# Optimization experiments

Measured on AMD Instinct MI355X. Metric: run time of the kernel, lower is better.

The kernel has to match this reference:

```python
import jax, jax.numpy as jnp
import numpy as np

D_IN, D_HID, D_CLS, N_CLASSES = 1024, 256, 128, 4
CELL_IN = 512
N = 50000


def setup_inputs() -> dict:
    key = jax.random.key(0)
    ks = jax.random.split(key, 20)
    s = 0.02
    inp = {
        "x_path": jax.random.normal(ks[0], (1, N, D_IN), jnp.float32),
        "x_cell": jax.random.normal(ks[1], (1, N, CELL_IN), jnp.float32),
        # wsi_net / cell_net projections
        "wsi_w": jax.random.normal(ks[2], (D_IN, D_HID), jnp.float32) * s,
        "wsi_b": jnp.zeros((D_HID,), jnp.float32),
        "cell_w": jax.random.normal(ks[3], (CELL_IN, D_HID), jnp.float32) * s,
        "cell_b": jnp.zeros((D_HID,), jnp.float32),
        # cross-attention Q/K/V
        "wq_w": jax.random.normal(ks[4], (D_HID, D_HID), jnp.float32) * s,
        "wq_b": jnp.zeros((D_HID,), jnp.float32),
        "wk_w": jax.random.normal(ks[5], (D_HID, D_HID), jnp.float32) * s,
        "wk_b": jnp.zeros((D_HID,), jnp.float32),
        "wv_w": jax.random.normal(ks[6], (D_HID, D_HID), jnp.float32) * s,
        "wv_b": jnp.zeros((D_HID,), jnp.float32),
        # gated attention (L=D=256, n_classes=1)
        "aa_w": jax.random.normal(ks[7], (D_HID, D_HID), jnp.float32) * s,
        "aa_b": jnp.zeros((D_HID,), jnp.float32),
        "ab_w": jax.random.normal(ks[8], (D_HID, D_HID), jnp.float32) * s,
        "ab_b": jnp.zeros((D_HID,), jnp.float32),
        "ac_w": jax.random.normal(ks[9], (D_HID, 1), jnp.float32) * s,
        "ac_b": jnp.zeros((1,), jnp.float32),
        # classifier MLP
        "c1_w": jax.random.normal(ks[10], (D_HID, D_CLS), jnp.float32) * s,
        "c1_b": jnp.zeros((D_CLS,), jnp.float32),
        "c2_w": jax.random.normal(ks[11], (D_CLS, N_CLASSES), jnp.float32) * s,
        "c2_b": jnp.zeros((N_CLASSES,), jnp.float32),
    }
    return inp


def reference(x_path, x_cell, wsi_w, wsi_b, cell_w, cell_b,
              wq_w, wq_b, wk_w, wk_b, wv_w, wv_b,
              aa_w, aa_b, ab_w, ab_b, ac_w, ac_b,
              c1_w, c1_b, c2_w, c2_b):
    xp = x_path[0]            # (N, D_IN)
    xc = x_cell[0]            # (N, CELL_IN)
    # instance-level projections (dropout inactive at eval)
    h_path = jax.nn.relu(xp @ wsi_w + wsi_b)    # (N, d)
    h_cell = jax.nn.relu(xc @ cell_w + cell_b)  # (N, d)
    # cross attention with per-instance seq_len=1 (bmm over N singleton batches)
    q = h_cell @ wq_w + wq_b
    k = h_path @ wk_w + wk_b
    v = h_path @ wv_w + wv_b
    scores = (jnp.einsum('nd,nd->n', q, k) / jnp.sqrt(jnp.float32(q.shape[-1])))[:, None, None]  # (N,1,1)
    attn_w = jax.nn.softmax(scores, axis=-1)     # (N,1,1), trivially ones
    fused = attn_w[:, 0, :] * v                  # (N, d)
    # gated attention MIL pooling
    a = jnp.tanh(fused @ aa_w + aa_b)
    b = jax.nn.sigmoid(fused @ ab_w + ab_b)
    A = (a * b) @ ac_w + ac_b                    # (N, 1)
    A_t = A.T                                    # (1, N)
    pooled = jax.nn.softmax(A_t, axis=1) @ fused # (1, d)
    # classifier MLP
    risk = jax.nn.relu(pooled @ c1_w + c1_b) @ c2_w + c2_b  # (1, n_classes)
    return risk
```

## Files before the change

### kernel.cpp

```cpp
#include <hip/hip_runtime.h>
#include <hip/hip_bf16.h>
#include <math.h>

#define D_IN 1024
#define D_HID 256
#define D_CLS 128
#define N_CLASSES 4
#define N_INST 50000

#define ROWS 64
#define NBLK ((N_INST + ROWS - 1) / ROWS)
#define NB2 64
#define CHUNK ((NBLK + NB2 - 1) / NB2)
#define NEG_BIG (-1e30f)

#define WS_W1T   0
#define WS_WVT   524288
#define WS_WAT   655360
#define WS_WBT   786432
#define WS_P1    917504
#define WS_P2    1724528
#define WS_XB    1835008
#define WS_NEED  (WS_XB + (size_t)N_INST * D_IN * 2)

typedef __attribute__((ext_vector_type(8))) short bf16x8;
typedef __attribute__((ext_vector_type(4))) float f32x4;

__device__ __forceinline__ short f2bf(float x) {
    __hip_bfloat16 h = __float2bfloat16(x);
    return *reinterpret_cast<short*>(&h);
}
__device__ __forceinline__ float fast_tanh(float x) {
    float e = __expf(2.f * x);
    return 1.f - 2.f * __builtin_amdgcn_rcpf(e + 1.f);
}
__device__ __forceinline__ float fast_sigmoid(float x) {
    return __builtin_amdgcn_rcpf(1.f + __expf(-x));
}
__device__ __forceinline__ bf16x8 load_cvt8(const float* __restrict__ p) {
    float4 a = *(const float4*)p;
    float4 b = *(const float4*)(p + 4);
    bf16x8 r;
    r[0] = f2bf(a.x); r[1] = f2bf(a.y); r[2] = f2bf(a.z); r[3] = f2bf(a.w);
    r[4] = f2bf(b.x); r[5] = f2bf(b.y); r[6] = f2bf(b.z); r[7] = f2bf(b.w);
    return r;
}

__global__ __launch_bounds__(256) void convert_x(const float* __restrict__ xp,
                                                 __hip_bfloat16* __restrict__ xb) {
    size_t i = ((size_t)blockIdx.x * 256 + threadIdx.x) * 8;
    bf16x8 v = load_cvt8(xp + i);
    *(bf16x8*)(xb + i) = v;
}

__global__ void convert_weights(const float* __restrict__ w1, const float* __restrict__ wv,
                                const float* __restrict__ wa, const float* __restrict__ wb,
                                __hip_bfloat16* __restrict__ w1t, __hip_bfloat16* __restrict__ wvt,
                                __hip_bfloat16* __restrict__ wat, __hip_bfloat16* __restrict__ wbt) {
    __shared__ __hip_bfloat16 T[64][68];
    int b = blockIdx.x, tid = threadIdx.x;
    const float* src; __hip_bfloat16* dst; int K, tr, tc;
    if (b < 64) { src = w1; dst = w1t; K = D_IN; tr = b >> 2; tc = b & 3; }
    else {
        int m = (b - 64) >> 4, t = (b - 64) & 15;
        src = (m == 0) ? wv : (m == 1) ? wa : wb;
        dst = (m == 0) ? wvt : (m == 1) ? wat : wbt;
        K = D_HID; tr = t >> 2; tc = t & 3;
    }
    int k0 = tr * 64, n0 = tc * 64;
#pragma unroll
    for (int p = 0; p < 4; p++) {
        int lin = p * 256 + tid;
        int r = lin >> 4;
        int c4 = (lin & 15) << 2;
        float4 v = *(const float4*)(src + (size_t)(k0 + r) * D_HID + n0 + c4);
        T[c4 + 0][r] = __float2bfloat16(v.x);
        T[c4 + 1][r] = __float2bfloat16(v.y);
        T[c4 + 2][r] = __float2bfloat16(v.z);
        T[c4 + 3][r] = __float2bfloat16(v.w);
    }
    __syncthreads();
#pragma unroll
    for (int p = 0; p < 4; p++) {
        int lin = p * 256 + tid;
        int n = lin >> 4;
        int kq = (lin & 15) << 2;
        ushort4 o;
        o.x = *(unsigned short*)&T[n][kq + 0];
        o.y = *(unsigned short*)&T[n][kq + 1];
        o.z = *(unsigned short*)&T[n][kq + 2];
        o.w = *(unsigned short*)&T[n][kq + 3];
        *(ushort4*)(dst + (size_t)(n0 + n) * K + k0 + kq) = o;
    }
}

__device__ __forceinline__ void gemm256_w8(const __hip_bfloat16 (*S)[264],
                                           const __hip_bfloat16* __restrict__ Wt,
                                           int colbase, int quad, int l16, f32x4 acc[4][2]) {
    f32x4 zero = {0.f, 0.f, 0.f, 0.f};
#pragma unroll
    for (int i = 0; i < 4; i++) { acc[i][0] = zero; acc[i][1] = zero; }
    const __hip_bfloat16* w0 = Wt + (size_t)(colbase + l16) * D_HID + quad * 8;
    const __hip_bfloat16* w1 = w0 + 16 * D_HID;
#pragma unroll
    for (int ks = 0; ks < 8; ks++) {
        bf16x8 af[4];
#pragma unroll
        for (int rt = 0; rt < 4; rt++)
            af[rt] = *(const bf16x8*)&S[rt * 16 + l16][ks * 32 + quad * 8];
        bf16x8 b0 = *(const bf16x8*)(w0 + ks * 32);
        bf16x8 b1 = *(const bf16x8*)(w1 + ks * 32);
#pragma unroll
        for (int rt = 0; rt < 4; rt++) {
            acc[rt][0] = __builtin_amdgcn_mfma_f32_16x16x32_bf16(af[rt], b0, acc[rt][0], 0, 0, 0);
            acc[rt][1] = __builtin_amdgcn_mfma_f32_16x16x32_bf16(af[rt], b1, acc[rt][1], 0, 0, 0);
        }
    }
}

template <bool XBF16>
__global__ __launch_bounds__(512, 4) void mcat_main(const void* __restrict__ xsrc,
                          const __hip_bfloat16* __restrict__ w1t, const float* __restrict__ b1,
                          const __hip_bfloat16* __restrict__ wvt, const float* __restrict__ bv,
                          const __hip_bfloat16* __restrict__ wat, const float* __restrict__ ba,
                          const __hip_bfloat16* __restrict__ wbt, const float* __restrict__ bb,
                          const float* __restrict__ acw, const float* __restrict__ acb,
                          float* __restrict__ partials) {
    __shared__ __hip_bfloat16 Hs[ROWS][264];
    __shared__ __hip_bfloat16 Vs[ROWS][264];
    __shared__ float Apart[8][ROWS];
    __shared__ float ExpW[ROWS];

    const int tid  = threadIdx.x;
    const int wave = tid >> 6;
    const int lane = tid & 63;
    const int quad = lane >> 4;
    const int l16  = lane & 15;
    const int colbase = wave * 32;
    const int row0 = blockIdx.x * ROWS;

    f32x4 acc[4][2];
    f32x4 zero = {0.f, 0.f, 0.f, 0.f};
#pragma unroll
    for (int i = 0; i < 4; i++) { acc[i][0] = zero; acc[i][1] = zero; }

    const __hip_bfloat16* xb_base[4];
    const float* xf_base[4];
#pragma unroll
    for (int rt = 0; rt < 4; rt++) {
        int r = row0 + rt * 16 + l16;
        if (r > N_INST - 1) r = N_INST - 1;
        if (XBF16) xb_base[rt] = (const __hip_bfloat16*)xsrc + (size_t)r * D_IN + quad * 8;
        else       xf_base[rt] = (const float*)xsrc + (size_t)r * D_IN + quad * 8;
    }
    const __hip_bfloat16* wb0 = w1t + (size_t)(colbase + l16) * D_IN + quad * 8;
    const __hip_bfloat16* wb1 = wb0 + 16 * D_IN;

    for (int kc = 0; kc < D_IN; kc += 32) {
        bf16x8 af[4];
#pragma unroll
        for (int rt = 0; rt < 4; rt++)
            af[rt] = XBF16 ? *(const bf16x8*)(xb_base[rt] + kc)
                           : load_cvt8(xf_base[rt] + kc);
        bf16x8 b0 = *(const bf16x8*)(wb0 + kc);
        bf16x8 b1 = *(const bf16x8*)(wb1 + kc);
#pragma unroll
        for (int rt = 0; rt < 4; rt++) {
            acc[rt][0] = __builtin_amdgcn_mfma_f32_16x16x32_bf16(af[rt], b0, acc[rt][0], 0, 0, 0);
            acc[rt][1] = __builtin_amdgcn_mfma_f32_16x16x32_bf16(af[rt], b1, acc[rt][1], 0, 0, 0);
        }
    }

#pragma unroll
    for (int ct = 0; ct < 2; ct++) {
        int col = colbase + ct * 16 + l16;
        float bias = b1[col];
#pragma unroll
        for (int rt = 0; rt < 4; rt++)
#pragma unroll
            for (int r = 0; r < 4; r++) {
                int row = rt * 16 + quad * 4 + r;
                Hs[row][col] = __float2bfloat16(fmaxf(acc[rt][ct][r] + bias, 0.f));
            }
    }
    __syncthreads();

    gemm256_w8(Hs, wvt, colbase, quad, l16, acc);
#pragma unroll
    for (int ct = 0; ct < 2; ct++) {
        int col = colbase + ct * 16 + l16;
        float bias = bv[col];
#pragma unroll
        for (int rt = 0; rt < 4; rt++)
#pragma unroll
            for (int r = 0; r < 4; r++) {
                int row = rt * 16 + quad * 4 + r;
                Vs[row][col] = __float2bfloat16(acc[rt][ct][r] + bias);
            }
    }
    __syncthreads();

    float a_reg[4][2][4];
    gemm256_w8(Vs, wat, colbase, quad, l16, acc);
#pragma unroll
    for (int ct = 0; ct < 2; ct++) {
        float bias = ba[colbase + ct * 16 + l16];
#pragma unroll
        for (int rt = 0; rt < 4; rt++)
#pragma unroll
            for (int r = 0; r < 4; r++)
                a_reg[rt][ct][r] = fast_tanh(acc[rt][ct][r] + bias);
    }

    gemm256_w8(Vs, wbt, colbase, quad, l16, acc);
    {
        float acw0 = acw[colbase + l16];
        float acw1 = acw[colbase + 16 + l16];
        float bias0 = bb[colbase + l16];
        float bias1 = bb[colbase + 16 + l16];
        float sp[4][4];
#pragma unroll
        for (int rt = 0; rt < 4; rt++)
#pragma unroll
            for (int r = 0; r < 4; r++) {
                float g0 = a_reg[rt][0][r] * fast_sigmoid(acc[rt][0][r] + bias0);
                float g1 = a_reg[rt][1][r] * fast_sigmoid(acc[rt][1][r] + bias1);
                sp[rt][r] = g0 * acw0 + g1 * acw1;
            }
#pragma unroll
        for (int off = 1; off < 16; off <<= 1)
#pragma unroll
            for (int rt = 0; rt < 4; rt++)
#pragma unroll
                for (int r = 0; r < 4; r++)
                    sp[rt][r] += __shfl_xor(sp[rt][r], off, 16);
        if (l16 == 0) {
#pragma unroll
            for (int rt = 0; rt < 4; rt++)
#pragma unroll
                for (int r = 0; r < 4; r++)
                    Apart[wave][rt * 16 + quad * 4 + r] = sp[rt][r];
        }
    }
    __syncthreads();

    if (tid < 64) {
        bool valid = (row0 + tid) < N_INST;
        float A = acb[0];
#pragma unroll
        for (int w = 0; w < 8; w++) A += Apart[w][tid];
        if (!valid) A = NEG_BIG;
        float m = A;
#pragma unroll
        for (int off = 32; off > 0; off >>= 1) m = fmaxf(m, __shfl_xor(m, off));
        float e = valid ? __expf(A - m) : 0.f;
        ExpW[tid] = e;
        float ssum = e;
#pragma unroll
        for (int off = 32; off > 0; off >>= 1) ssum += __shfl_xor(ssum, off);
        if (tid == 0) {
            partials[(size_t)blockIdx.x * 258 + 0] = m;
            partials[(size_t)blockIdx.x * 258 + 1] = ssum;
        }
    }
    __syncthreads();
    if (tid < 256) {
        float p = 0.f;
#pragma unroll 8
        for (int n = 0; n < 64; n++)
            p += ExpW[n] * __bfloat162float(Vs[n][tid]);
        partials[(size_t)blockIdx.x * 258 + 2 + tid] = p;
    }
}

__global__ void mcat_fin_a(const float* __restrict__ p1, float* __restrict__ p2) {
    __shared__ float sm[1];
    int g = blockIdx.x, tid = threadIdx.x;
    int lo = g * CHUNK;
    int hi = lo + CHUNK; if (hi > NBLK) hi = NBLK;
    if (tid < 64) {
        float m = NEG_BIG;
        if (lo + tid < hi) m = p1[(size_t)(lo + tid) * 258];
#pragma unroll
        for (int off = 32; off > 0; off >>= 1) m = fmaxf(m, __shfl_xor(m, off));
        if (tid == 0) sm[0] = m;
    }
    __syncthreads();
    float M = sm[0];
    float p = 0.f, sacc = 0.f;
    for (int b = lo; b < hi; b++) {
        float sc = __expf(p1[(size_t)b * 258] - M);
        sacc += sc * p1[(size_t)b * 258 + 1];
        p += sc * p1[(size_t)b * 258 + 2 + tid];
    }
    if (tid == 0) {
        p2[(size_t)g * 258 + 0] = M;
        p2[(size_t)g * 258 + 1] = sacc;
    }
    p2[(size_t)g * 258 + 2 + tid] = p;
}

__global__ void mcat_fin_b(const float* __restrict__ p2,
                           const float* __restrict__ c1w, const float* __restrict__ c1b,
                           const float* __restrict__ c2w, const float* __restrict__ c2b,
                           float* __restrict__ out) {
    __shared__ float sm[2];
    __shared__ float sc[NB2];
    __shared__ float pooled[D_HID];
    __shared__ float r1[D_CLS];
    int tid = threadIdx.x;
    if (tid < 64) {
        float m = p2[(size_t)tid * 258];
#pragma unroll
        for (int off = 32; off > 0; off >>= 1) m = fmaxf(m, __shfl_xor(m, off));
        if (tid == 0) sm[0] = m;
    }
    __syncthreads();
    float M = sm[0];
    if (tid < 64) {
        float s = __expf(p2[(size_t)tid * 258] - M);
        sc[tid] = s;
        float Ssum = s * p2[(size_t)tid * 258 + 1];
#pragma unroll
        for (int off = 32; off > 0; off >>= 1) Ssum += __shfl_xor(Ssum, off);
        if (tid == 0) sm[1] = Ssum;
    }
    __syncthreads();
    float S = sm[1];
    float p = 0.f;
#pragma unroll 8
    for (int b = 0; b < NB2; b++)
        p += sc[b] * p2[(size_t)b * 258 + 2 + tid];
    pooled[tid] = p / S;
    __syncthreads();
    if (tid < D_CLS) {
        float acc = c1b[tid];
#pragma unroll 8
        for (int d = 0; d < D_HID; d++)
            acc += pooled[d] * c1w[(size_t)d * D_CLS + tid];
        r1[tid] = fmaxf(acc, 0.f);
    }
    __syncthreads();
    if (tid < N_CLASSES) {
        float acc = c2b[tid];
#pragma unroll 8
        for (int j = 0; j < D_CLS; j++)
            acc += r1[j] * c2w[(size_t)j * N_CLASSES + tid];
        out[tid] = acc;
    }
}

extern "C" void kernel_launch(void* const* d_in, const int* in_sizes, int n_in,
                              void* d_out, int out_size, void* d_ws, size_t ws_size,
                              hipStream_t stream) {
    const float* xp  = (const float*)d_in[0];
    const float* w1  = (const float*)d_in[2];
    const float* b1  = (const float*)d_in[3];
    const float* wv  = (const float*)d_in[10];
    const float* bv  = (const float*)d_in[11];
    const float* wa  = (const float*)d_in[12];
    const float* ba  = (const float*)d_in[13];
    const float* wb  = (const float*)d_in[14];
    const float* bb  = (const float*)d_in[15];
    const float* acw = (const float*)d_in[16];
    const float* acb = (const float*)d_in[17];
    const float* c1w = (const float*)d_in[18];
    const float* c1b = (const float*)d_in[19];
    const float* c2w = (const float*)d_in[20];
    const float* c2b = (const float*)d_in[21];
    float* out = (float*)d_out;

    char* ws = (char*)d_ws;
    __hip_bfloat16* w1t = (__hip_bfloat16*)(ws + WS_W1T);
    __hip_bfloat16* wvt = (__hip_bfloat16*)(ws + WS_WVT);
    __hip_bfloat16* wat = (__hip_bfloat16*)(ws + WS_WAT);
    __hip_bfloat16* wbt = (__hip_bfloat16*)(ws + WS_WBT);
    float* p1 = (float*)(ws + WS_P1);
    float* p2 = (float*)(ws + WS_P2);
    __hip_bfloat16* xb = (__hip_bfloat16*)(ws + WS_XB);

    const bool big = ws_size >= WS_NEED;

    hipLaunchKernelGGL(convert_weights, dim3(112), dim3(256), 0, stream,
                       w1, wv, wa, wb, w1t, wvt, wat, wbt);
    if (big) {
        hipLaunchKernelGGL(convert_x, dim3(N_INST * D_IN / 8 / 256), dim3(256), 0, stream, xp, xb);
        hipLaunchKernelGGL((mcat_main<true>), dim3(NBLK), dim3(512), 0, stream,
                           (const void*)xb, w1t, b1, wvt, bv, wat, ba, wbt, bb, acw, acb, p1);
    } else {
        hipLaunchKernelGGL((mcat_main<false>), dim3(NBLK), dim3(512), 0, stream,
                           (const void*)xp, w1t, b1, wvt, bv, wat, ba, wbt, bb, acw, acb, p1);
    }
    hipLaunchKernelGGL(mcat_fin_a, dim3(NB2), dim3(256), 0, stream, p1, p2);
    hipLaunchKernelGGL(mcat_fin_b, dim3(1), dim3(256), 0, stream,
                       p2, c1w, c1b, c2w, c2b, out);
}
```

Baseline: 623.9 us.

## Split pipeline into fp32-input GEMM stage and fused attention stage with last-block finalize

Drops the separate fp32-to-bf16 conversion pass over x. A new stage1 kernel reads fp32 x directly, caches a 64-column slice of W1 in LDS and double-buffers the global loads, then writes a bf16 hidden matrix. A stage2 kernel runs the V/gate GEMMs on 128-row tiles and performs the final softmax reduction and classifier in the last block, using an atomic counter. This replaces the two finalize launches and avoids the extra full-size x write and read, at the cost of a bf16 hidden-activation round trip through memory.

```diff
diff --git a/kernel.cpp b/kernel.cpp
--- a/kernel.cpp
+++ b/kernel.cpp
@@ -8,20 +8,31 @@
 #define N_CLASSES 4
 #define N_INST 50000
 
+#define RG1 512
+#define CG1 64
+#define NPAD 50176
+#define GA (NPAD / RG1 * 4)
+#define RG2 128
+#define GB (NPAD / RG2)
+#define PSTR 258
+
 #define ROWS 64
 #define NBLK ((N_INST + ROWS - 1) / ROWS)
 #define NB2 64
 #define CHUNK ((NBLK + NB2 - 1) / NB2)
 #define NEG_BIG (-1e30f)
 
-#define WS_W1T   0
-#define WS_WVT   524288
-#define WS_WAT   655360
-#define WS_WBT   786432
-#define WS_P1    917504
-#define WS_P2    1724528
-#define WS_XB    1835008
-#define WS_NEED  (WS_XB + (size_t)N_INST * D_IN * 2)
+#define WS_W1T   0u
+#define WS_WVT   524288u
+#define WS_WAT   655360u
+#define WS_WBT   786432u
+#define WS_CNT   917504u
+#define WS_P1    917760u
+#define WS_H     1322304u
+#define WS_NEED2 (WS_H + (size_t)NPAD * D_HID * 2)
+#define WS_P1F   917504u
+#define WS_P2F   1724800u
+#define WS_NEEDF (WS_P2F + 66048u)
 
 typedef __attribute__((ext_vector_type(8))) short bf16x8;
 typedef __attribute__((ext_vector_type(4))) float f32x4;
@@ -37,20 +48,14 @@
 __device__ __forceinline__ float fast_sigmoid(float x) {
     return __builtin_amdgcn_rcpf(1.f + __expf(-x));
 }
-__device__ __forceinline__ bf16x8 load_cvt8(const float* __restrict__ p) {
-    float4 a = *(const float4*)p;
-    float4 b = *(const float4*)(p + 4);
+__device__ __forceinline__ bf16x8 cvt8(float4 a, float4 b) {
     bf16x8 r;
     r[0] = f2bf(a.x); r[1] = f2bf(a.y); r[2] = f2bf(a.z); r[3] = f2bf(a.w);
     r[4] = f2bf(b.x); r[5] = f2bf(b.y); r[6] = f2bf(b.z); r[7] = f2bf(b.w);
     return r;
 }
-
-__global__ __launch_bounds__(256) void convert_x(const float* __restrict__ xp,
-                                                 __hip_bfloat16* __restrict__ xb) {
-    size_t i = ((size_t)blockIdx.x * 256 + threadIdx.x) * 8;
-    bf16x8 v = load_cvt8(xp + i);
-    *(bf16x8*)(xb + i) = v;
+__device__ __forceinline__ bf16x8 load_cvt8(const float* __restrict__ p) {
+    return cvt8(*(const float4*)p, *(const float4*)(p + 4));
 }
 
 __global__ void convert_weights(const float* __restrict__ w1, const float* __restrict__ wv,
@@ -94,6 +99,345 @@
     }
 }
 
+union Smem1 {
+    __hip_bfloat16 W[CG1][1032];
+    __hip_bfloat16 O[RG1][72];
+};
+
+__global__ __launch_bounds__(512, 2) void mcat_stage1(const float* __restrict__ xp,
+                                                      const __hip_bfloat16* __restrict__ w1t,
+                                                      const float* __restrict__ b1,
+                                                      __hip_bfloat16* __restrict__ hout) {
+    __shared__ Smem1 sm;
+    const int tid  = threadIdx.x;
+    const int wave = tid >> 6;
+    const int lane = tid & 63;
+    const int quad = lane >> 4;
+    const int l16  = lane & 15;
+    const int colg = blockIdx.x & 3;
+    const int rowg = blockIdx.x >> 2;
+    const int col0 = colg * CG1;
+    const int row0 = rowg * RG1;
+
+    {
+        int c  = tid >> 3;
+        int k0 = (tid & 7) * 8;
+        const __hip_bfloat16* src = w1t + (size_t)(col0 + c) * D_IN;
+#pragma unroll
+        for (int j = 0; j < 16; j++)
+            *(bf16x8*)&sm.W[c][k0 + j * 64] = *(const bf16x8*)(src + k0 + j * 64);
+    }
+    __syncthreads();
+
+    const float* xrow[4];
+#pragma unroll
+    for (int rt = 0; rt < 4; rt++) {
+        int r = row0 + wave * 64 + rt * 16 + l16;
+        if (r > N_INST - 1) r = N_INST - 1;
+        xrow[rt] = xp + (size_t)r * D_IN + quad * 8;
+    }
+
+    f32x4 acc[4][4];
+    f32x4 zero = {0.f, 0.f, 0.f, 0.f};
+#pragma unroll
+    for (int i = 0; i < 4; i++)
+#pragma unroll
+        for (int j = 0; j < 4; j++) acc[i][j] = zero;
+
+    float4 buf[2][4][2];
+#pragma unroll
+    for (int rt = 0; rt < 4; rt++) {
+        buf[0][rt][0] = *(const float4*)(xrow[rt]);
+        buf[0][rt][1] = *(const float4*)(xrow[rt] + 4);
+    }
+#pragma unroll
+    for (int kc = 0; kc < 32; kc++) {
+        const int ph = kc & 1;
+        if (kc < 31) {
+#pragma unroll
+            for (int rt = 0; rt < 4; rt++) {
+                buf[ph ^ 1][rt][0] = *(const float4*)(xrow[rt] + (kc + 1) * 32);
+                buf[ph ^ 1][rt][1] = *(const float4*)(xrow[rt] + (kc + 1) * 32 + 4);
+            }
+        }
+        bf16x8 af[4];
+#pragma unroll
+        for (int rt = 0; rt < 4; rt++)
+            af[rt] = cvt8(buf[ph][rt][0], buf[ph][rt][1]);
+        bf16x8 bfr[4];
+#pragma unroll
+        for (int ct = 0; ct < 4; ct++)
+            bfr[ct] = *(const bf16x8*)&sm.W[ct * 16 + l16][kc * 32 + quad * 8];
+#pragma unroll
+        for (int ct = 0; ct < 4; ct++)
+#pragma unroll
+            for (int rt = 0; rt < 4; rt++)
+                acc[rt][ct] = __builtin_amdgcn_mfma_f32_16x16x32_bf16(af[rt], bfr[ct], acc[rt][ct], 0, 0, 0);
+    }
+
+    __syncthreads();
+#pragma unroll
+    for (int ct = 0; ct < 4; ct++) {
+        float bias = b1[col0 + ct * 16 + l16];
+#pragma unroll
+        for (int rt = 0; rt < 4; rt++)
+#pragma unroll
+            for (int r = 0; r < 4; r++) {
+                int row = wave * 64 + rt * 16 + quad * 4 + r;
+                sm.O[row][ct * 16 + l16] = __float2bfloat16(fmaxf(acc[rt][ct][r] + bias, 0.f));
+            }
+    }
+    __syncthreads();
+    {
+        __hip_bfloat16* d = hout + (size_t)(row0 + tid) * D_HID + col0;
+#pragma unroll
+        for (int j = 0; j < 8; j++)
+            *(bf16x8*)(d + j * 8) = *(const bf16x8*)&sm.O[tid][j * 8];
+    }
+}
+
+__global__ __launch_bounds__(512, 2) void mcat_stage2(const __hip_bfloat16* __restrict__ h,
+                          const __hip_bfloat16* __restrict__ wvt, const float* __restrict__ bv,
+                          const __hip_bfloat16* __restrict__ wat, const float* __restrict__ ba,
+                          const __hip_bfloat16* __restrict__ wbt, const float* __restrict__ bb,
+                          const float* __restrict__ acw, const float* __restrict__ acb,
+                          float* __restrict__ p1, unsigned int* __restrict__ counter,
+                          const float* __restrict__ c1w, const float* __restrict__ c1b,
+                          const float* __restrict__ c2w, const float* __restrict__ c2b,
+                          float* __restrict__ out) {
+    __shared__ __hip_bfloat16 Hs[RG2][264];
+    __shared__ __hip_bfloat16 Vs[RG2][264];
+    __shared__ float Apart[8][RG2];
+    __shared__ float ExpW[RG2];
+    __shared__ float smx[4];
+
+    const int tid  = threadIdx.x;
+    const int wave = tid >> 6;
+    const int lane = tid & 63;
+    const int quad = lane >> 4;
+    const int l16  = lane & 15;
+    const int cb   = wave * 32;
+    const int row0 = blockIdx.x * RG2;
+
+    {
+        int r = tid >> 2;
+        int k0 = (tid & 3) * 8;
+#pragma unroll
+        for (int j = 0; j < 8; j++)
+            *(bf16x8*)&Hs[r][k0 + j * 32] = *(const bf16x8*)(h + (size_t)(row0 + r) * D_HID + k0 + j * 32);
+    }
+    __syncthreads();
+
+    f32x4 acc[8][2];
+    f32x4 zero = {0.f, 0.f, 0.f, 0.f};
+
+#pragma unroll
+    for (int i = 0; i < 8; i++) { acc[i][0] = zero; acc[i][1] = zero; }
+    {
+        const __hip_bfloat16* w0 = wvt + (size_t)(cb + l16) * D_HID + quad * 8;
+        const __hip_bfloat16* w1p = w0 + 16 * D_HID;
+#pragma unroll
+        for (int ks = 0; ks < 8; ks++) {
+            bf16x8 b0 = *(const bf16x8*)(w0 + ks * 32);
+            bf16x8 b1f = *(const bf16x8*)(w1p + ks * 32);
+#pragma unroll
+            for (int rt = 0; rt < 8; rt++) {
+                bf16x8 af = *(const bf16x8*)&Hs[rt * 16 + l16][ks * 32 + quad * 8];
+                acc[rt][0] = __builtin_amdgcn_mfma_f32_16x16x32_bf16(af, b0, acc[rt][0], 0, 0, 0);
+                acc[rt][1] = __builtin_amdgcn_mfma_f32_16x16x32_bf16(af, b1f, acc[rt][1], 0, 0, 0);
+            }
+        }
+    }
+#pragma unroll
+    for (int ct = 0; ct < 2; ct++) {
+        int col = cb + ct * 16 + l16;
+        float bias = bv[col];
+#pragma unroll
+        for (int rt = 0; rt < 8; rt++)
+#pragma unroll
+            for (int r = 0; r < 4; r++)
+                Vs[rt * 16 + quad * 4 + r][col] = __float2bfloat16(acc[rt][ct][r] + bias);
+    }
+    __syncthreads();
+
+    float a_reg[8][2][4];
+#pragma unroll
+    for (int i = 0; i < 8; i++) { acc[i][0] = zero; acc[i][1] = zero; }
+    {
+        const __hip_bfloat16* w0 = wat + (size_t)(cb + l16) * D_HID + quad * 8;
+        const __hip_bfloat16* w1p = w0 + 16 * D_HID;
+#pragma unroll
+        for (int ks = 0; ks < 8; ks++) {
+            bf16x8 b0 = *(const bf16x8*)(w0 + ks * 32);
+            bf16x8 b1f = *(const bf16x8*)(w1p + ks * 32);
+#pragma unroll
+            for (int rt = 0; rt < 8; rt++) {
+                bf16x8 af = *(const bf16x8*)&Vs[rt * 16 + l16][ks * 32 + quad * 8];
+                acc[rt][0] = __builtin_amdgcn_mfma_f32_16x16x32_bf16(af, b0, acc[rt][0], 0, 0, 0);
+                acc[rt][1] = __builtin_amdgcn_mfma_f32_16x16x32_bf16(af, b1f, acc[rt][1], 0, 0, 0);
+            }
+        }
+    }
+#pragma unroll
+    for (int ct = 0; ct < 2; ct++) {
+        float bias = ba[cb + ct * 16 + l16];
+#pragma unroll
+        for (int rt = 0; rt < 8; rt++)
+#pragma unroll
+            for (int r = 0; r < 4; r++)
+                a_reg[rt][ct][r] = fast_tanh(acc[rt][ct][r] + bias);
+    }
+
+#pragma unroll
+    for (int i = 0; i < 8; i++) { acc[i][0] = zero; acc[i][1] = zero; }
+    {
+        const __hip_bfloat16* w0 = wbt + (size_t)(cb + l16) * D_HID + quad * 8;
+        const __hip_bfloat16* w1p = w0 + 16 * D_HID;
+#pragma unroll
+        for (int ks = 0; ks < 8; ks++) {
+            bf16x8 b0 = *(const bf16x8*)(w0 + ks * 32);
+            bf16x8 b1f = *(const bf16x8*)(w1p + ks * 32);
+#pragma unroll
+            for (int rt = 0; rt < 8; rt++) {
+                bf16x8 af = *(const bf16x8*)&Vs[rt * 16 + l16][ks * 32 + quad * 8];
+                acc[rt][0] = __builtin_amdgcn_mfma_f32_16x16x32_bf16(af, b0, acc[rt][0], 0, 0, 0);
+                acc[rt][1] = __builtin_amdgcn_mfma_f32_16x16x32_bf16(af, b1f, acc[rt][1], 0, 0, 0);
+            }
+        }
+    }
+    {
+        float acw0 = acw[cb + l16], acw1 = acw[cb + 16 + l16];
+        float bb0 = bb[cb + l16],  bb1 = bb[cb + 16 + l16];
+        float sp[8][4];
+#pragma unroll
+        for (int rt = 0; rt < 8; rt++)
+#pragma unroll
+            for (int r = 0; r < 4; r++) {
+                float g0 = a_reg[rt][0][r] * fast_sigmoid(acc[rt][0][r] + bb0);
+                float g1 = a_reg[rt][1][r] * fast_sigmoid(acc[rt][1][r] + bb1);
+                sp[rt][r] = g0 * acw0 + g1 * acw1;
+            }
+#pragma unroll
+        for (int off = 1; off < 16; off <<= 1)
+#pragma unroll
+            for (int rt = 0; rt < 8; rt++)
+#pragma unroll
+                for (int r = 0; r < 4; r++)
+                    sp[rt][r] += __shfl_xor(sp[rt][r], off, 16);
+        if (l16 == 0) {
+#pragma unroll
+            for (int rt = 0; rt < 8; rt++)
+#pragma unroll
+                for (int r = 0; r < 4; r++)
+                    Apart[wave][rt * 16 + quad * 4 + r] = sp[rt][r];
+        }
+    }
+    __syncthreads();
+
+    if (tid < 64) {
+        float A0 = acb[0], A1 = acb[0];
+#pragma unroll
+        for (int w = 0; w < 8; w++) { A0 += Apart[w][tid]; A1 += Apart[w][tid + 64]; }
+        bool v0 = (row0 + tid) < N_INST;
+        bool v1 = (row0 + 64 + tid) < N_INST;
+        if (!v0) A0 = NEG_BIG;
+        if (!v1) A1 = NEG_BIG;
+        float m = fmaxf(A0, A1);
+#pragma unroll
+        for (int off = 32; off > 0; off >>= 1) m = fmaxf(m, __shfl_xor(m, off));
+        float e0 = v0 ? __expf(A0 - m) : 0.f;
+        float e1 = v1 ? __expf(A1 - m) : 0.f;
+        ExpW[tid] = e0; ExpW[tid + 64] = e1;
+        float ssum = e0 + e1;
+#pragma unroll
+        for (int off = 32; off > 0; off >>= 1) ssum += __shfl_xor(ssum, off);
+        if (tid == 0) {
+            p1[(size_t)blockIdx.x * PSTR + 0] = m;
+            p1[(size_t)blockIdx.x * PSTR + 1] = ssum;
+        }
+    }
+    __syncthreads();
+    if (tid < 256) {
+        float p = 0.f;
+#pragma unroll 8
+        for (int n = 0; n < RG2; n++)
+            p += ExpW[n] * __bfloat162float(Vs[n][tid]);
+        p1[(size_t)blockIdx.x * PSTR + 2 + tid] = p;
+    }
+
+    __syncthreads();
+    if (tid == 0) {
+        __threadfence();
+        unsigned int old = __hip_atomic_fetch_add(counter, 1u, __ATOMIC_ACQ_REL, __HIP_MEMORY_SCOPE_AGENT);
+        smx[3] = (old == GB - 1) ? 1.f : 0.f;
+    }
+    __syncthreads();
+    if (smx[3] == 0.f) return;
+    __threadfence();
+
+    float* sc     = (float*)Hs;
+    float* pooled = (float*)Vs;
+    float* r1     = pooled + 256;
+
+    {
+        float mloc = NEG_BIG;
+        for (int b = tid; b < GB; b += 512) mloc = fmaxf(mloc, p1[(size_t)b * PSTR]);
+#pragma unroll
+        for (int off = 32; off > 0; off >>= 1) mloc = fmaxf(mloc, __shfl_xor(mloc, off));
+        if (lane == 0) ExpW[wave] = mloc;
+    }
+    __syncthreads();
+    if (tid == 0) {
+        float M = NEG_BIG;
+#pragma unroll
+        for (int w = 0; w < 8; w++) M = fmaxf(M, ExpW[w]);
+        smx[0] = M;
+    }
+    __syncthreads();
+    {
+        float M = smx[0];
+        float sl = 0.f;
+        for (int b = tid; b < GB; b += 512) {
+            float scb = __expf(p1[(size_t)b * PSTR] - M);
+            sc[b] = scb;
+            sl += scb * p1[(size_t)b * PSTR + 1];
+        }
+#pragma unroll
+        for (int off = 32; off > 0; off >>= 1) sl += __shfl_xor(sl, off);
+        if (lane == 0) ExpW[8 + wave] = sl;
+    }
+    __syncthreads();
+    if (tid == 0) {
+        float S = 0.f;
+#pragma unroll
+        for (int w = 0; w < 8; w++) S += ExpW[8 + w];
+        smx[1] = S;
+    }
+    __syncthreads();
+    if (tid < 256) {
+        float p = 0.f;
+        for (int b = 0; b < GB; b++)
+            p += sc[b] * p1[(size_t)b * PSTR + 2 + tid];
+        pooled[tid] = p / smx[1];
+    }
+    __syncthreads();
+    if (tid < D_CLS) {
+        float a2 = c1b[tid];
+#pragma unroll 8
+        for (int d = 0; d < D_HID; d++)
+            a2 += pooled[d] * c1w[(size_t)d * D_CLS + tid];
+        r1[tid] = fmaxf(a2, 0.f);
+    }
+    __syncthreads();
+    if (tid < N_CLASSES) {
+        float a2 = c2b[tid];
+#pragma unroll 8
+        for (int j = 0; j < D_CLS; j++)
+            a2 += r1[j] * c2w[(size_t)j * N_CLASSES + tid];
+        out[tid] = a2;
+    }
+}
+
 __device__ __forceinline__ void gemm256_w8(const __hip_bfloat16 (*S)[264],
                                            const __hip_bfloat16* __restrict__ Wt,
                                            int colbase, int quad, int l16, f32x4 acc[4][2]) {
@@ -118,8 +462,7 @@
     }
 }
 
-template <bool XBF16>
-__global__ __launch_bounds__(512, 4) void mcat_main(const void* __restrict__ xsrc,
+__global__ __launch_bounds__(512, 4) void mcat_mainF(const float* __restrict__ xsrc,
                           const __hip_bfloat16* __restrict__ w1t, const float* __restrict__ b1,
                           const __hip_bfloat16* __restrict__ wvt, const float* __restrict__ bv,
                           const __hip_bfloat16* __restrict__ wat, const float* __restrict__ ba,
@@ -130,7 +473,6 @@
     __shared__ __hip_bfloat16 Vs[ROWS][264];
     __shared__ float Apart[8][ROWS];
     __shared__ float ExpW[ROWS];
-
     const int tid  = threadIdx.x;
     const int wave = tid >> 6;
     const int lane = tid & 63;
@@ -138,30 +480,23 @@
     const int l16  = lane & 15;
     const int colbase = wave * 32;
     const int row0 = blockIdx.x * ROWS;
-
     f32x4 acc[4][2];
     f32x4 zero = {0.f, 0.f, 0.f, 0.f};
 #pragma unroll
     for (int i = 0; i < 4; i++) { acc[i][0] = zero; acc[i][1] = zero; }
-
-    const __hip_bfloat16* xb_base[4];
     const float* xf_base[4];
 #pragma unroll
     for (int rt = 0; rt < 4; rt++) {
         int r = row0 + rt * 16 + l16;
         if (r > N_INST - 1) r = N_INST - 1;
-        if (XBF16) xb_base[rt] = (const __hip_bfloat16*)xsrc + (size_t)r * D_IN + quad * 8;
-        else       xf_base[rt] = (const float*)xsrc + (size_t)r * D_IN + quad * 8;
+        xf_base[rt] = xsrc + (size_t)r * D_IN + quad * 8;
     }
     const __hip_bfloat16* wb0 = w1t + (size_t)(colbase + l16) * D_IN + quad * 8;
     const __hip_bfloat16* wb1 = wb0 + 16 * D_IN;
-
     for (int kc = 0; kc < D_IN; kc += 32) {
         bf16x8 af[4];
 #pragma unroll
-        for (int rt = 0; rt < 4; rt++)
-            af[rt] = XBF16 ? *(const bf16x8*)(xb_base[rt] + kc)
-                           : load_cvt8(xf_base[rt] + kc);
+        for (int rt = 0; rt < 4; rt++) af[rt] = load_cvt8(xf_base[rt] + kc);
         bf16x8 b0 = *(const bf16x8*)(wb0 + kc);
         bf16x8 b1 = *(const bf16x8*)(wb1 + kc);
 #pragma unroll
@@ -170,7 +505,6 @@
             acc[rt][1] = __builtin_amdgcn_mfma_f32_16x16x32_bf16(af[rt], b1, acc[rt][1], 0, 0, 0);
         }
     }
-
 #pragma unroll
     for (int ct = 0; ct < 2; ct++) {
         int col = colbase + ct * 16 + l16;
@@ -178,13 +512,10 @@
 #pragma unroll
         for (int rt = 0; rt < 4; rt++)
 #pragma unroll
-            for (int r = 0; r < 4; r++) {
-                int row = rt * 16 + quad * 4 + r;
-                Hs[row][col] = __float2bfloat16(fmaxf(acc[rt][ct][r] + bias, 0.f));
-            }
-    }
-    __syncthreads();
-
+            for (int r = 0; r < 4; r++)
+                Hs[rt * 16 + quad * 4 + r][col] = __float2bfloat16(fmaxf(acc[rt][ct][r] + bias, 0.f));
+    }
+    __syncthreads();
     gemm256_w8(Hs, wvt, colbase, quad, l16, acc);
 #pragma unroll
     for (int ct = 0; ct < 2; ct++) {
@@ -193,13 +524,10 @@
 #pragma unroll
         for (int rt = 0; rt < 4; rt++)
 #pragma unroll
-            for (int r = 0; r < 4; r++) {
-                int row = rt * 16 + quad * 4 + r;
-                Vs[row][col] = __float2bfloat16(acc[rt][ct][r] + bias);
-            }
-    }
-    __syncthreads();
-
+            for (int r = 0; r < 4; r++)
+                Vs[rt * 16 + quad * 4 + r][col] = __float2bfloat16(acc[rt][ct][r] + bias);
+    }
+    __syncthreads();
     float a_reg[4][2][4];
     gemm256_w8(Vs, wat, colbase, quad, l16, acc);
 #pragma unroll
@@ -211,7 +539,6 @@
             for (int r = 0; r < 4; r++)
                 a_reg[rt][ct][r] = fast_tanh(acc[rt][ct][r] + bias);
     }
-
     gemm256_w8(Vs, wbt, colbase, quad, l16, acc);
     {
         float acw0 = acw[colbase + l16];
@@ -243,7 +570,6 @@
         }
     }
     __syncthreads();
-
     if (tid < 64) {
         bool valid = (row0 + tid) < N_INST;
         float A = acb[0];
@@ -259,8 +585,8 @@
 #pragma unroll
         for (int off = 32; off > 0; off >>= 1) ssum += __shfl_xor(ssum, off);
         if (tid == 0) {
-            partials[(size_t)blockIdx.x * 258 + 0] = m;
-            partials[(size_t)blockIdx.x * 258 + 1] = ssum;
+            partials[(size_t)blockIdx.x * PSTR + 0] = m;
+            partials[(size_t)blockIdx.x * PSTR + 1] = ssum;
         }
     }
     __syncthreads();
@@ -269,7 +595,7 @@
 #pragma unroll 8
         for (int n = 0; n < 64; n++)
             p += ExpW[n] * __bfloat162float(Vs[n][tid]);
-        partials[(size_t)blockIdx.x * 258 + 2 + tid] = p;
+        partials[(size_t)blockIdx.x * PSTR + 2 + tid] = p;
     }
 }
 
@@ -280,7 +606,7 @@
     int hi = lo + CHUNK; if (hi > NBLK) hi = NBLK;
     if (tid < 64) {
         float m = NEG_BIG;
-        if (lo + tid < hi) m = p1[(size_t)(lo + tid) * 258];
+        if (lo + tid < hi) m = p1[(size_t)(lo + tid) * PSTR];
 #pragma unroll
         for (int off = 32; off > 0; off >>= 1) m = fmaxf(m, __shfl_xor(m, off));
         if (tid == 0) sm[0] = m;
@@ -289,15 +615,15 @@
     float M = sm[0];
     float p = 0.f, sacc = 0.f;
     for (int b = lo; b < hi; b++) {
-        float sc = __expf(p1[(size_t)b * 258] - M);
-        sacc += sc * p1[(size_t)b * 258 + 1];
-        p += sc * p1[(size_t)b * 258 + 2 + tid];
+        float sc = __expf(p1[(size_t)b * PSTR] - M);
+        sacc += sc * p1[(size_t)b * PSTR + 1];
+        p += sc * p1[(size_t)b * PSTR + 2 + tid];
     }
     if (tid == 0) {
-        p2[(size_t)g * 258 + 0] = M;
-        p2[(size_t)g * 258 + 1] = sacc;
-    }
-    p2[(size_t)g * 258 + 2 + tid] = p;
+        p2[(size_t)g * PSTR + 0] = M;
+        p2[(size_t)g * PSTR + 1] = sacc;
+    }
+    p2[(size_t)g * PSTR + 2 + tid] = p;
 }
 
 __global__ void mcat_fin_b(const float* __restrict__ p2,
@@ -310,7 +636,7 @@
     __shared__ float r1[D_CLS];
     int tid = threadIdx.x;
     if (tid < 64) {
-        float m = p2[(size_t)tid * 258];
+        float m = p2[(size_t)tid * PSTR];
 #pragma unroll
         for (int off = 32; off > 0; off >>= 1) m = fmaxf(m, __shfl_xor(m, off));
         if (tid == 0) sm[0] = m;
@@ -318,9 +644,9 @@
     __syncthreads();
     float M = sm[0];
     if (tid < 64) {
-        float s = __expf(p2[(size_t)tid * 258] - M);
+        float s = __expf(p2[(size_t)tid * PSTR] - M);
         sc[tid] = s;
-        float Ssum = s * p2[(size_t)tid * 258 + 1];
+        float Ssum = s * p2[(size_t)tid * PSTR + 1];
 #pragma unroll
         for (int off = 32; off > 0; off >>= 1) Ssum += __shfl_xor(Ssum, off);
         if (tid == 0) sm[1] = Ssum;
@@ -330,7 +656,7 @@
     float p = 0.f;
 #pragma unroll 8
     for (int b = 0; b < NB2; b++)
-        p += sc[b] * p2[(size_t)b * 258 + 2 + tid];
+        p += sc[b] * p2[(size_t)b * PSTR + 2 + tid];
     pooled[tid] = p / S;
     __syncthreads();
     if (tid < D_CLS) {
@@ -375,23 +701,26 @@
     __hip_bfloat16* wvt = (__hip_bfloat16*)(ws + WS_WVT);
     __hip_bfloat16* wat = (__hip_bfloat16*)(ws + WS_WAT);
     __hip_bfloat16* wbt = (__hip_bfloat16*)(ws + WS_WBT);
-    float* p1 = (float*)(ws + WS_P1);
-    float* p2 = (float*)(ws + WS_P2);
-    __hip_bfloat16* xb = (__hip_bfloat16*)(ws + WS_XB);
-
-    const bool big = ws_size >= WS_NEED;
 
     hipLaunchKernelGGL(convert_weights, dim3(112), dim3(256), 0, stream,
                        w1, wv, wa, wb, w1t, wvt, wat, wbt);
-    if (big) {
-        hipLaunchKernelGGL(convert_x, dim3(N_INST * D_IN / 8 / 256), dim3(256), 0, stream, xp, xb);
-        hipLaunchKernelGGL((mcat_main<true>), dim3(NBLK), dim3(512), 0, stream,
-                           (const void*)xb, w1t, b1, wvt, bv, wat, ba, wbt, bb, acw, acb, p1);
+
+    if (ws_size >= WS_NEED2) {
+        unsigned int* counter = (unsigned int*)(ws + WS_CNT);
+        float* p1 = (float*)(ws + WS_P1);
+        __hip_bfloat16* h = (__hip_bfloat16*)(ws + WS_H);
+        hipMemsetAsync(counter, 0, 4, stream);
+        hipLaunchKernelGGL(mcat_stage1, dim3(GA), dim3(512), 0, stream, xp, w1t, b1, h);
+        hipLaunchKernelGGL(mcat_stage2, dim3(GB), dim3(512), 0, stream,
+                           h, wvt, bv, wat, ba, wbt, bb, acw, acb, p1, counter,
+                           c1w, c1b, c2w, c2b, out);
     } else {
-        hipLaunchKernelGGL((mcat_main<false>), dim3(NBLK), dim3(512), 0, stream,
-                           (const void*)xp, w1t, b1, wvt, bv, wat, ba, wbt, bb, acw, acb, p1);
-    }
-    hipLaunchKernelGGL(mcat_fin_a, dim3(NB2), dim3(256), 0, stream, p1, p2);
-    hipLaunchKernelGGL(mcat_fin_b, dim3(1), dim3(256), 0, stream,
-                       p2, c1w, c1b, c2w, c2b, out);
-}
+        float* p1 = (float*)(ws + WS_P1F);
+        float* p2 = (float*)(ws + WS_P2F);
+        hipLaunchKernelGGL(mcat_mainF, dim3(NBLK), dim3(512), 0, stream,
+                           xp, w1t, b1, wvt, bv, wat, ba, wbt, bb, acw, acb, p1);
+        hipLaunchKernelGGL(mcat_fin_a, dim3(NB2), dim3(256), 0, stream, p1, p2);
+        hipLaunchKernelGGL(mcat_fin_b, dim3(1), dim3(256), 0, stream,
+                           p2, c1w, c1b, c2w, c2b, out);
+    }
+}
```

Result: slower. 652.4 us (+4.6%).
